# Kernel tuning notes

Hardware: AMD Instinct MI355X
Metric: run time of the kernel (lower is better)

The kernel has to match this reference:

```python
import jax, jax.numpy as jnp
import numpy as np

D = 1024
DFF = 4096  # SwiGLU hidden = 4*d_model
EPS = 1e-6

def rmsnorm(x, w):
    return x * jax.lax.rsqrt(jnp.mean(x * x, axis=-1, keepdims=True) + EPS) * w

def mingru_scan(gates, cands):
    # h_t = g_t * h_{t-1} + (1 - g_t) * c_t, h_0 = 0 -> linear recurrence,
    # solved with an associative scan over pairs (a, b): h = a*h_prev + b.
    a = gates
    b = (1.0 - gates) * cands
    def combine(e1, e2):
        a1, b1 = e1
        a2, b2 = e2
        return (a1 * a2, a2 * b1 + b2)
    _, h = jax.lax.associative_scan(combine, (a, b), axis=1)
    return h

def setup_inputs() -> dict:
    key = jax.random.key(0)
    ks = jax.random.split(key, 10)
    xavier = lambda k, fan_in, fan_out: jax.random.uniform(
        k, (fan_in, fan_out), jnp.float32,
        -np.sqrt(6.0 / (fan_in + fan_out)), np.sqrt(6.0 / (fan_in + fan_out)))
    return {
        "x": jax.random.normal(ks[0], (4, 4096, D), jnp.float32),
        "Wg": xavier(ks[1], D, D),
        "bg": jnp.ones((D,), jnp.float32),   # gate bias init = 1.0
        "Wc": xavier(ks[2], D, D),
        "bc": jnp.zeros((D,), jnp.float32),
        "n1_w": jnp.ones((D,), jnp.float32),
        "n2_w": jnp.ones((D,), jnp.float32),
        "W1": xavier(ks[3], D, DFF),   # SwiGLU gate proj
        "W3": xavier(ks[4], D, DFF),   # SwiGLU up proj
        "W2": xavier(ks[5], DFF, D),   # SwiGLU down proj
    }

def reference(x, Wg, bg, Wc, bc, n1_w, n2_w, W1, W3, W2):
    # --- MinGRU sub-block (pre-norm, residual) ---
    h_in = rmsnorm(x, n1_w)
    gates = jax.nn.sigmoid(jnp.einsum('bld,de->ble', h_in, Wg) + bg)
    cands = jnp.tanh(jnp.einsum('bld,de->ble', h_in, Wc) + bc)
    x = x + mingru_scan(gates, cands)
    # --- SwiGLU FFN sub-block (pre-norm, residual) ---
    f_in = rmsnorm(x, n2_w)
    ff = jnp.einsum('blf,fd->bld',
                    jax.nn.silu(jnp.einsum('bld,df->blf', f_in, W1))
                    * jnp.einsum('bld,df->blf', f_in, W3), W2)
    return x + ff
```

## Files before the change

### kernel.cpp

```cpp
#include <hip/hip_runtime.h>
#include <hip/hip_bf16.h>
#include <math.h>

typedef __bf16 bf16_t;
typedef bf16_t bf16x8 __attribute__((ext_vector_type(8)));
typedef bf16_t bf16x4 __attribute__((ext_vector_type(4)));
typedef bf16_t bf16x2 __attribute__((ext_vector_type(2)));
typedef float f32x4 __attribute__((ext_vector_type(4)));

#define D_MODEL 1024
#define SEQ     4096
#define BATCH   4
#define NTOK    16384
#define DFF     4096
#define CLEN    64
#define NCHUNK  64
#define NCH     4096

__device__ __forceinline__ void gload16(const bf16_t* g, bf16_t* l) {
    __builtin_amdgcn_global_load_lds(
        (const __attribute__((address_space(1))) void*)g,
        (__attribute__((address_space(3))) void*)l, 16, 0, 0);
}

__global__ void transpose_to_bf16(const float* __restrict__ W,
                                  bf16_t* __restrict__ Wt, int R, int C) {
    __shared__ float tile[32][33];
    const int c0 = blockIdx.x * 32, r0 = blockIdx.y * 32;
    const int tx = threadIdx.x, ty = threadIdx.y;
#pragma unroll
    for (int j = 0; j < 32; j += 8)
        tile[ty + j][tx] = W[(size_t)(r0 + ty + j) * C + c0 + tx];
    __syncthreads();
#pragma unroll
    for (int j = 0; j < 32; j += 8)
        Wt[(size_t)(c0 + ty + j) * R + r0 + tx] = (bf16_t)tile[tx][ty + j];
}

__global__ void rmsnorm_kernel(const float* __restrict__ x,
                               const float* __restrict__ w,
                               bf16_t* __restrict__ out) {
    const int row = blockIdx.x;
    const int tid = threadIdx.x;
    const float4 v = ((const float4*)(x + (size_t)row * D_MODEL))[tid];
    float ss = v.x * v.x + v.y * v.y + v.z * v.z + v.w * v.w;
#pragma unroll
    for (int o = 1; o < 64; o <<= 1) ss += __shfl_xor(ss, o);
    __shared__ float red[4];
    if ((tid & 63) == 0) red[tid >> 6] = ss;
    __syncthreads();
    const float tot = red[0] + red[1] + red[2] + red[3];
    const float scale = rsqrtf(tot * (1.0f / D_MODEL) + 1e-6f);
    const float4 wv = ((const float4*)w)[tid];
    bf16x4 o4;
    o4[0] = (bf16_t)(v.x * scale * wv.x);
    o4[1] = (bf16_t)(v.y * scale * wv.y);
    o4[2] = (bf16_t)(v.z * scale * wv.z);
    o4[3] = (bf16_t)(v.w * scale * wv.w);
    ((bf16x4*)(out + (size_t)row * D_MODEL))[tid] = o4;
}

#define MFMA16(a, b, c) __builtin_amdgcn_mfma_f32_16x16x32_bf16((a), (b), (c), 0, 0, 0)

template <int MODE>
__global__ __launch_bounds__(512, 2)
void gemm8p(const bf16_t* __restrict__ A, const bf16_t* __restrict__ B1t,
            const bf16_t* __restrict__ B2t, const float* __restrict__ bias1,
            const float* __restrict__ bias2, bf16x2* __restrict__ GC,
            bf16_t* __restrict__ Ot, float* __restrict__ O,
            int N, int K, int lg_nbn) {
    constexpr bool DUAL = (MODE != 2);
    constexpr int BN = DUAL ? 128 : 256;
    constexpr int NFR = DUAL ? 2 : 4;
    constexpr int NMAT = DUAL ? 2 : 1;
    __shared__ bf16_t lds[65536];

    const int tid = threadIdx.x;
    const int lane = tid & 63;
    const int wave = tid >> 6;
    const int wr = wave >> 2, wc = wave & 3;
    const int lr16 = lane & 15, lk = lane >> 4;

    const int nwg = gridDim.x;
    const int wg = blockIdx.x;
    const int swg = (wg & 7) * (nwg >> 3) + (wg >> 3);
    const int bn = swg & ((1 << lg_nbn) - 1);
    const int bm = swg >> lg_nbn;
    const int nt = K >> 6;

    const int lr8 = lane >> 3;
    const int cge = ((lane & 7) ^ lr8) << 3;
    const bf16_t* Ag  = A   + (size_t)(bm * 256 + wave * 8 + lr8) * K + cge;
    const bf16_t* B1g = B1t + (size_t)(bn * BN  + wave * 8 + lr8) * K + cge;
    const bf16_t* B2g = DUAL ? (B2t + (size_t)(bn * BN + wave * 8 + lr8) * K + cge)
                             : (const bf16_t*)nullptr;

    f32x4 acc1[8][NFR] = {};
    f32x4 acc2[DUAL ? 8 : 1][NFR] = {};

    auto stageA = [&](int u) {
        bf16_t* dst = &lds[(u & 1) * 32768 + wave * 512];
        const bf16_t* src = Ag + ((size_t)u << 6);
        gload16(src,                     dst);
        gload16(src + ((size_t)64  * K), dst + 4096);
        gload16(src + ((size_t)128 * K), dst + 8192);
        gload16(src + ((size_t)192 * K), dst + 12288);
    };
    auto stageB = [&](int u) {
        bf16_t* dst = &lds[(u & 1) * 32768 + 16384 + wave * 512];
        const bf16_t* src = B1g + ((size_t)u << 6);
        gload16(src,                    dst);
        gload16(src + ((size_t)64 * K), dst + 4096);
        if constexpr (DUAL) {
            bf16_t* dst2 = &lds[(u & 1) * 32768 + 24576 + wave * 512];
            const bf16_t* src2 = B2g + ((size_t)u << 6);
            gload16(src2,                    dst2);
            gload16(src2 + ((size_t)64 * K), dst2 + 4096);
        } else {
            gload16(src + ((size_t)128 * K), dst + 8192);
            gload16(src + ((size_t)192 * K), dst + 12288);
        }
    };
    auto rdA = [&](int p, int m, int ks) {
        const int row = wr * 128 + m * 16 + lr16;
        const int c = ks * 4 + lk;
        return *(const bf16x8*)&lds[p * 32768 + row * 64 + (((c ^ row) & 7) << 3)];
    };
    auto rdB = [&](int p, int mat, int n, int ks) {
        const int row = wc * (BN / 4) + n * 16 + lr16;
        const int c = ks * 4 + lk;
        return *(const bf16x8*)&lds[p * 32768 + 16384 + mat * 8192 + row * 64 +
                                    (((c ^ row) & 7) << 3)];
    };

    stageA(0);
    stageB(0);
    stageA(1);
    asm volatile("s_waitcnt vmcnt(4)" ::: "memory");
    __builtin_amdgcn_s_barrier();

    for (int t = 0; t < nt; ++t) {
        const int p = t & 1;
        bf16x8 bF[NMAT][NFR];
        bf16x8 aF[4];

#pragma unroll
        for (int mat = 0; mat < NMAT; ++mat)
#pragma unroll
            for (int n = 0; n < NFR; ++n) bF[mat][n] = rdB(p, mat, n, 0);
#pragma unroll
        for (int m = 0; m < 4; ++m) aF[m] = rdA(p, m, 0);
        if (t + 1 < nt) stageB(t + 1);
        __builtin_amdgcn_s_barrier();
        asm volatile("s_waitcnt lgkmcnt(0)" ::: "memory");
        __builtin_amdgcn_sched_barrier(0);
        __builtin_amdgcn_s_setprio(1);
#pragma unroll
        for (int m = 0; m < 4; ++m)
#pragma unroll
            for (int n = 0; n < NFR; ++n) {
                acc1[m][n] = MFMA16(aF[m], bF[0][n], acc1[m][n]);
                if constexpr (DUAL) acc2[m][n] = MFMA16(aF[m], bF[1][n], acc2[m][n]);
            }
        __builtin_amdgcn_s_setprio(0);
        __builtin_amdgcn_s_barrier();

#pragma unroll
        for (int m = 0; m < 4; ++m) aF[m] = rdA(p, 4 + m, 0);
        __builtin_amdgcn_s_barrier();
        asm volatile("s_waitcnt lgkmcnt(0)" ::: "memory");
        __builtin_amdgcn_sched_barrier(0);
        __builtin_amdgcn_s_setprio(1);
#pragma unroll
        for (int m = 0; m < 4; ++m)
#pragma unroll
            for (int n = 0; n < NFR; ++n) {
                acc1[4 + m][n] = MFMA16(aF[m], bF[0][n], acc1[4 + m][n]);
                if constexpr (DUAL) acc2[4 + m][n] = MFMA16(aF[m], bF[1][n], acc2[4 + m][n]);
            }
        __builtin_amdgcn_s_setprio(0);
        __builtin_amdgcn_s_barrier();

#pragma unroll
        for (int mat = 0; mat < NMAT; ++mat)
#pragma unroll
            for (int n = 0; n < NFR; ++n) bF[mat][n] = rdB(p, mat, n, 1);
#pragma unroll
        for (int m = 0; m < 4; ++m) aF[m] = rdA(p, m, 1);
        __builtin_amdgcn_s_barrier();
        asm volatile("s_waitcnt lgkmcnt(0)" ::: "memory");
        __builtin_amdgcn_sched_barrier(0);
        __builtin_amdgcn_s_setprio(1);
#pragma unroll
        for (int m = 0; m < 4; ++m)
#pragma unroll
            for (int n = 0; n < NFR; ++n) {
                acc1[m][n] = MFMA16(aF[m], bF[0][n], acc1[m][n]);
                if constexpr (DUAL) acc2[m][n] = MFMA16(aF[m], bF[1][n], acc2[m][n]);
            }
        __builtin_amdgcn_s_setprio(0);
        __builtin_amdgcn_s_barrier();

#pragma unroll
        for (int m = 0; m < 4; ++m) aF[m] = rdA(p, 4 + m, 1);
        asm volatile("s_waitcnt lgkmcnt(0)" ::: "memory");
        __builtin_amdgcn_s_barrier();
        if (t + 2 < nt) stageA(t + 2);
        __builtin_amdgcn_sched_barrier(0);
        __builtin_amdgcn_s_setprio(1);
#pragma unroll
        for (int m = 0; m < 4; ++m)
#pragma unroll
            for (int n = 0; n < NFR; ++n) {
                acc1[4 + m][n] = MFMA16(aF[m], bF[0][n], acc1[4 + m][n]);
                if constexpr (DUAL) acc2[4 + m][n] = MFMA16(aF[m], bF[1][n], acc2[4 + m][n]);
            }
        __builtin_amdgcn_s_setprio(0);
        __builtin_amdgcn_sched_barrier(0);
        if (t + 2 < nt) {
            asm volatile("s_waitcnt vmcnt(4)" ::: "memory");
        } else {
            asm volatile("s_waitcnt vmcnt(0)" ::: "memory");
        }
        __builtin_amdgcn_s_barrier();
    }

    const int rowBase = bm * 256 + wr * 128;
    const int colBase = bn * BN + wc * (BN / 4);
#pragma unroll
    for (int n = 0; n < NFR; ++n) {
        const int col = colBase + n * 16 + lr16;
        float b1v = 0.f, b2v = 0.f;
        if constexpr (MODE == 0) { b1v = bias1[col]; b2v = bias2[col]; }
#pragma unroll
        for (int m = 0; m < 8; ++m) {
#pragma unroll
            for (int j = 0; j < 4; ++j) {
                const int row = rowBase + m * 16 + lk * 4 + j;
                const size_t idx = (size_t)row * N + col;
                if constexpr (MODE == 0) {
                    const float gv = 1.0f / (1.0f + __expf(-(acc1[m][n][j] + b1v)));
                    const float cv = tanhf(acc2[m][n][j] + b2v);
                    bf16x2 pk;
                    pk[0] = (bf16_t)gv;
                    pk[1] = (bf16_t)cv;
                    GC[idx] = pk;
                } else if constexpr (MODE == 1) {
                    const float a = acc1[m][n][j];
                    const float s = a / (1.0f + __expf(-a));
                    Ot[idx] = (bf16_t)(s * acc2[m][n][j]);
                } else {
                    O[idx] += acc1[m][n][j];
                }
            }
        }
    }
}

__global__ void scan_phase1(const bf16x2* __restrict__ gc,
                            float* __restrict__ cA, float* __restrict__ cB) {
    const int d = blockIdx.x * 256 + threadIdx.x;
    const int b = blockIdx.y;
    const int cidx = blockIdx.z;
    const int ch = b * D_MODEL + d;
    const size_t base = ((size_t)b * SEQ + (size_t)cidx * CLEN) * D_MODEL + d;
    float A = 1.0f, Bv = 0.0f;
#pragma unroll 8
    for (int t = 0; t < CLEN; ++t) {
        const bf16x2 v = gc[base + (size_t)t * D_MODEL];
        const float gv = (float)v[0], cv = (float)v[1];
        Bv = gv * Bv + (1.0f - gv) * cv;
        A *= gv;
    }
    cA[cidx * NCH + ch] = A;
    cB[cidx * NCH + ch] = Bv;
}

__global__ void scan_phase2(const float* __restrict__ cA,
                            const float* __restrict__ cB,
                            float* __restrict__ hstart) {
    const int ch = blockIdx.x * 256 + threadIdx.x;
    float h = 0.0f;
#pragma unroll 8
    for (int cdx = 0; cdx < NCHUNK; ++cdx) {
        hstart[cdx * NCH + ch] = h;
        h = cA[cdx * NCH + ch] * h + cB[cdx * NCH + ch];
    }
}

__global__ void scan_phase3(const bf16x2* __restrict__ gc,
                            const float* __restrict__ hstart,
                            const float* __restrict__ x,
                            float* __restrict__ x1) {
    const int d = blockIdx.x * 256 + threadIdx.x;
    const int b = blockIdx.y;
    const int cidx = blockIdx.z;
    const int ch = b * D_MODEL + d;
    const size_t base = ((size_t)b * SEQ + (size_t)cidx * CLEN) * D_MODEL + d;
    float h = hstart[cidx * NCH + ch];
#pragma unroll 8
    for (int t = 0; t < CLEN; ++t) {
        const size_t off = base + (size_t)t * D_MODEL;
        const bf16x2 v = gc[off];
        const float gv = (float)v[0], cv = (float)v[1];
        h = gv * h + (1.0f - gv) * cv;
        x1[off] = x[off] + h;
    }
}

extern "C" void kernel_launch(void* const* d_in, const int* in_sizes, int n_in,
                              void* d_out, int out_size, void* d_ws,
                              size_t ws_size, hipStream_t stream) {
    const float* x   = (const float*)d_in[0];
    const float* Wg  = (const float*)d_in[1];
    const float* bg  = (const float*)d_in[2];
    const float* Wc  = (const float*)d_in[3];
    const float* bc  = (const float*)d_in[4];
    const float* n1w = (const float*)d_in[5];
    const float* n2w = (const float*)d_in[6];
    const float* W1  = (const float*)d_in[7];
    const float* W3  = (const float*)d_in[8];
    const float* W2  = (const float*)d_in[9];
    float* out = (float*)d_out;

    char* p = (char*)d_ws;
    bf16_t* tbuf  = (bf16_t*)p;
    bf16_t* h_in  = (bf16_t*)p;  p += (size_t)NTOK * D_MODEL * 2;
    bf16x2* gcbuf = (bf16x2*)p;  p += (size_t)NTOK * D_MODEL * 4;
    p += (size_t)32 << 20;
    bf16_t* f_in  = (bf16_t*)p;  p += (size_t)NTOK * D_MODEL * 2;
    bf16_t* Wg_t  = (bf16_t*)p;  p += (size_t)D_MODEL * D_MODEL * 2;
    bf16_t* Wc_t  = (bf16_t*)p;  p += (size_t)D_MODEL * D_MODEL * 2;
    bf16_t* W1_t  = (bf16_t*)p;  p += (size_t)DFF * D_MODEL * 2;
    bf16_t* W3_t  = (bf16_t*)p;  p += (size_t)DFF * D_MODEL * 2;
    bf16_t* W2_t  = (bf16_t*)p;  p += (size_t)D_MODEL * DFF * 2;
    float* cA     = (float*)p;   p += (size_t)NCHUNK * NCH * 4;
    float* cB     = (float*)p;   p += (size_t)NCHUNK * NCH * 4;
    float* hstart = (float*)p;   p += (size_t)NCHUNK * NCH * 4;

    const dim3 tb(32, 8);
    transpose_to_bf16<<<dim3(1024 / 32, 1024 / 32), tb, 0, stream>>>(Wg, Wg_t, 1024, 1024);
    transpose_to_bf16<<<dim3(1024 / 32, 1024 / 32), tb, 0, stream>>>(Wc, Wc_t, 1024, 1024);
    transpose_to_bf16<<<dim3(4096 / 32, 1024 / 32), tb, 0, stream>>>(W1, W1_t, 1024, 4096);
    transpose_to_bf16<<<dim3(4096 / 32, 1024 / 32), tb, 0, stream>>>(W3, W3_t, 1024, 4096);
    transpose_to_bf16<<<dim3(1024 / 32, 4096 / 32), tb, 0, stream>>>(W2, W2_t, 4096, 1024);

    rmsnorm_kernel<<<NTOK, 256, 0, stream>>>(x, n1w, h_in);

    gemm8p<0><<<512, 512, 0, stream>>>(h_in, Wg_t, Wc_t, bg, bc, gcbuf,
                                       nullptr, nullptr, D_MODEL, D_MODEL, 3);

    scan_phase1<<<dim3(D_MODEL / 256, BATCH, NCHUNK), 256, 0, stream>>>(gcbuf, cA, cB);
    scan_phase2<<<NCH / 256, 256, 0, stream>>>(cA, cB, hstart);
    scan_phase3<<<dim3(D_MODEL / 256, BATCH, NCHUNK), 256, 0, stream>>>(gcbuf, hstart, x, out);

    rmsnorm_kernel<<<NTOK, 256, 0, stream>>>(out, n2w, f_in);

    gemm8p<1><<<2048, 512, 0, stream>>>(f_in, W1_t, W3_t, nullptr, nullptr,
                                        nullptr, tbuf, nullptr, DFF, D_MODEL, 5);

    gemm8p<2><<<256, 512, 0, stream>>>(tbuf, W2_t, nullptr, nullptr, nullptr,
                                       nullptr, nullptr, out, D_MODEL, DFF, 2);
}
```

Measured before the change: 761.8 us.

## Precompute swizzled LDS addresses, unroll by two, split B staging across phases

LDS read addresses, including the XOR swizzle, are now computed once before the loop. The main loop is unrolled by two so each ping-pong buffer uses constant base offsets, which removes per-iteration address arithmetic. The next tile's B load is split into two halves issued in separate compute phases, spreading global-to-LDS traffic more evenly across the iteration. This assumes nt is even and changes the order in which vmcnt counts are retired, so the existing waitcnt values must still cover the split loads.

```diff
diff --git a/kernel.cpp b/kernel.cpp
--- a/kernel.cpp
+++ b/kernel.cpp
@@ -95,6 +95,15 @@
     const bf16_t* B2g = DUAL ? (B2t + (size_t)(bn * BN + wave * 8 + lr8) * K + cge)
                              : (const bf16_t*)nullptr;
 
+    const int swzE0 = (lk ^ (lr16 & 7)) * 8;
+    const int swzE1 = ((4 + lk) ^ (lr16 & 7)) * 8;
+    const int aBaseE = (wr * 128 + lr16) * 64;
+    const int bBaseE = (wc * (BN / 4) + lr16) * 64 + 16384;
+    const int aA0_0 = aBaseE + swzE0,         aA1_0 = aBaseE + swzE1;
+    const int bA0_0 = bBaseE + swzE0,         bA1_0 = bBaseE + swzE1;
+    const int aA0_1 = aA0_0 + 32768,          aA1_1 = aA1_0 + 32768;
+    const int bA0_1 = bA0_0 + 32768,          bA1_1 = bA1_0 + 32768;
+
     f32x4 acc1[8][NFR] = {};
     f32x4 acc2[DUAL ? 8 : 1][NFR] = {};
 
@@ -106,51 +115,54 @@
         gload16(src + ((size_t)128 * K), dst + 8192);
         gload16(src + ((size_t)192 * K), dst + 12288);
     };
-    auto stageB = [&](int u) {
+    auto stageBhalf = [&](int u, int h) {
         bf16_t* dst = &lds[(u & 1) * 32768 + 16384 + wave * 512];
         const bf16_t* src = B1g + ((size_t)u << 6);
-        gload16(src,                    dst);
-        gload16(src + ((size_t)64 * K), dst + 4096);
         if constexpr (DUAL) {
-            bf16_t* dst2 = &lds[(u & 1) * 32768 + 24576 + wave * 512];
-            const bf16_t* src2 = B2g + ((size_t)u << 6);
-            gload16(src2,                    dst2);
-            gload16(src2 + ((size_t)64 * K), dst2 + 4096);
+            if (h == 0) {
+                gload16(src,                    dst);
+                gload16(src + ((size_t)64 * K), dst + 4096);
+            } else {
+                bf16_t* dst2 = dst + 8192;
+                const bf16_t* src2 = B2g + ((size_t)u << 6);
+                gload16(src2,                    dst2);
+                gload16(src2 + ((size_t)64 * K), dst2 + 4096);
+            }
         } else {
-            gload16(src + ((size_t)128 * K), dst + 8192);
-            gload16(src + ((size_t)192 * K), dst + 12288);
+            if (h == 0) {
+                gload16(src,                    dst);
+                gload16(src + ((size_t)64 * K), dst + 4096);
+            } else {
+                gload16(src + ((size_t)128 * K), dst + 8192);
+                gload16(src + ((size_t)192 * K), dst + 12288);
+            }
         }
     };
-    auto rdA = [&](int p, int m, int ks) {
-        const int row = wr * 128 + m * 16 + lr16;
-        const int c = ks * 4 + lk;
-        return *(const bf16x8*)&lds[p * 32768 + row * 64 + (((c ^ row) & 7) << 3)];
-    };
-    auto rdB = [&](int p, int mat, int n, int ks) {
-        const int row = wc * (BN / 4) + n * 16 + lr16;
-        const int c = ks * 4 + lk;
-        return *(const bf16x8*)&lds[p * 32768 + 16384 + mat * 8192 + row * 64 +
-                                    (((c ^ row) & 7) << 3)];
+    auto rdA2 = [&](int adr, int m) {
+        return *(const bf16x8*)&lds[adr + m * 1024];
+    };
+    auto rdB2 = [&](int adr, int mat, int n) {
+        return *(const bf16x8*)&lds[adr + mat * 8192 + n * 1024];
     };
 
     stageA(0);
-    stageB(0);
+    stageBhalf(0, 0);
+    stageBhalf(0, 1);
     stageA(1);
     asm volatile("s_waitcnt vmcnt(4)" ::: "memory");
     __builtin_amdgcn_s_barrier();
 
-    for (int t = 0; t < nt; ++t) {
-        const int p = t & 1;
+    auto body = [&](int t, int aA0, int aA1, int bA0, int bA1) {
         bf16x8 bF[NMAT][NFR];
         bf16x8 aF[4];
 
 #pragma unroll
         for (int mat = 0; mat < NMAT; ++mat)
 #pragma unroll
-            for (int n = 0; n < NFR; ++n) bF[mat][n] = rdB(p, mat, n, 0);
-#pragma unroll
-        for (int m = 0; m < 4; ++m) aF[m] = rdA(p, m, 0);
-        if (t + 1 < nt) stageB(t + 1);
+            for (int n = 0; n < NFR; ++n) bF[mat][n] = rdB2(bA0, mat, n);
+#pragma unroll
+        for (int m = 0; m < 4; ++m) aF[m] = rdA2(aA0, m);
+        if (t + 1 < nt) stageBhalf(t + 1, 0);
         __builtin_amdgcn_s_barrier();
         asm volatile("s_waitcnt lgkmcnt(0)" ::: "memory");
         __builtin_amdgcn_sched_barrier(0);
@@ -166,7 +178,8 @@
         __builtin_amdgcn_s_barrier();
 
 #pragma unroll
-        for (int m = 0; m < 4; ++m) aF[m] = rdA(p, 4 + m, 0);
+        for (int m = 0; m < 4; ++m) aF[m] = rdA2(aA0, 4 + m);
+        if (t + 1 < nt) stageBhalf(t + 1, 1);
         __builtin_amdgcn_s_barrier();
         asm volatile("s_waitcnt lgkmcnt(0)" ::: "memory");
         __builtin_amdgcn_sched_barrier(0);
@@ -184,9 +197,9 @@
 #pragma unroll
         for (int mat = 0; mat < NMAT; ++mat)
 #pragma unroll
-            for (int n = 0; n < NFR; ++n) bF[mat][n] = rdB(p, mat, n, 1);
-#pragma unroll
-        for (int m = 0; m < 4; ++m) aF[m] = rdA(p, m, 1);
+            for (int n = 0; n < NFR; ++n) bF[mat][n] = rdB2(bA1, mat, n);
+#pragma unroll
+        for (int m = 0; m < 4; ++m) aF[m] = rdA2(aA1, m);
         __builtin_amdgcn_s_barrier();
         asm volatile("s_waitcnt lgkmcnt(0)" ::: "memory");
         __builtin_amdgcn_sched_barrier(0);
@@ -202,7 +215,7 @@
         __builtin_amdgcn_s_barrier();
 
 #pragma unroll
-        for (int m = 0; m < 4; ++m) aF[m] = rdA(p, 4 + m, 1);
+        for (int m = 0; m < 4; ++m) aF[m] = rdA2(aA1, 4 + m);
         asm volatile("s_waitcnt lgkmcnt(0)" ::: "memory");
         __builtin_amdgcn_s_barrier();
         if (t + 2 < nt) stageA(t + 2);
@@ -223,6 +236,11 @@
             asm volatile("s_waitcnt vmcnt(0)" ::: "memory");
         }
         __builtin_amdgcn_s_barrier();
+    };
+
+    for (int t = 0; t < nt; t += 2) {
+        body(t,     aA0_0, aA1_0, bA0_0, bA1_0);
+        body(t + 1, aA0_1, aA1_1, bA0_1, bA1_1);
     }
 
     const int rowBase = bm * 256 + wr * 128;
```

Measured after the change: 770.7 us. Within noise of the previous version (+1.2%).
